# Performance work log

Measured on AMD Instinct MI355X. Metric: run time of the kernel, lower is better.

The kernel has to match this reference:

```python
import jax, jax.numpy as jnp
import numpy as np


def setup_inputs() -> dict:
    key = jax.random.key(0)
    k1, k2, k3 = jax.random.split(key, 3)
    B, N, D = 4, 256, 128
    s = jax.random.normal(k1, (B, N, D), dtype=jnp.float32)
    W1 = jax.random.normal(k2, (3 * D, 2 * D), dtype=jnp.float32) * 0.02
    b1 = jnp.zeros((2 * D,), dtype=jnp.float32)
    W2 = jax.random.normal(k3, (2 * D, 1), dtype=jnp.float32) * 0.02
    b2 = jnp.zeros((1,), dtype=jnp.float32)
    return {"s": s, "W1": W1, "b1": b1, "W2": W2, "b2": b2, "K": 8}


def reference(s, W1, b1, W2, b2, K):
    B, N, D = s.shape
    si = jnp.broadcast_to(s[:, :, None, :], (B, N, N, D))
    sj = jnp.broadcast_to(s[:, None, :, :], (B, N, N, D))
    pair = jnp.concatenate([si, sj, si * sj], axis=-1)  # [B,N,N,3D]
    h = jax.nn.relu(pair @ W1 + b1)                      # [B,N,N,2D]
    scores = (h @ W2 + b2)[..., 0]                       # [B,N,N]
    k = min(int(K), N)
    _, idx = jax.lax.top_k(scores, k)                    # [B,N,K]
    # scatter ones at topk indices (indices are distinct per row)
    gate = jnp.sum(jax.nn.one_hot(idx, N, dtype=jnp.float32), axis=-2)  # [B,N,N]
    w = gate / jnp.clip(jnp.sum(gate, axis=-1, keepdims=True), 1.0)
    ctx = jnp.einsum('bij,bjd->bid', w, s)               # [B,N,D]
    return ctx, gate, w
```

## Files before the change

kernel.cpp:

```cpp
#include <hip/hip_runtime.h>
#include <hip/hip_bf16.h>
#include <math.h>

#define B_ 4
#define N_ 256
#define D_ 128
#define H_ 256
#define K_ 8

typedef __attribute__((ext_vector_type(8))) short short8;
typedef __attribute__((ext_vector_type(4))) float f32x4;

__device__ __forceinline__ unsigned short f2bf(float x) {
    union { __hip_bfloat16 h; unsigned short s; } u;
    u.h = __float2bfloat16(x);
    return u.s;
}
__device__ __forceinline__ float bf2f(unsigned short b) {
    unsigned v = ((unsigned)b) << 16;
    return __builtin_bit_cast(float, v);
}
__device__ __forceinline__ unsigned pk2(float x, float y) {
    union { __hip_bfloat162 h; unsigned u; } c;
    c.h = __float22bfloat162_rn(float2{x, y});
    return c.u;
}
__device__ __forceinline__ void gld_lds16(const float* g, float* l) {
    __builtin_amdgcn_global_load_lds(
        (const __attribute__((address_space(1))) void*)g,
        (__attribute__((address_space(3))) void*)l, 16, 0, 0);
}

__global__ __launch_bounds__(256) void pre_kernel(
    const float* __restrict__ s, const float* __restrict__ W1,
    const float* __restrict__ b1,
    float* __restrict__ avec, float* __restrict__ bvec,
    unsigned short* __restrict__ Wt)
{
    int blk = blockIdx.x;
    int t = threadIdx.x;
    if (blk < 512) {
        int bi0 = blk * 2;
        __shared__ float s2[2][D_];
        {
            int r = t >> 7, d = t & 127;
            s2[r][d] = s[(size_t)(bi0 + r) * D_ + d];
        }
        __syncthreads();
        float aA0 = b1[t], aA1 = aA0, aB0 = 0.f, aB1 = 0.f;
        const float* W1a = W1 + t;
        const float* W1b = W1 + (size_t)D_ * H_ + t;
        #pragma unroll 8
        for (int d = 0; d < D_; ++d) {
            float wa = W1a[(size_t)d * H_];
            float wb = W1b[(size_t)d * H_];
            float s0 = s2[0][d], s1 = s2[1][d];
            aA0 = fmaf(s0, wa, aA0);
            aA1 = fmaf(s1, wa, aA1);
            aB0 = fmaf(s0, wb, aB0);
            aB1 = fmaf(s1, wb, aB1);
        }
        avec[(size_t)bi0 * H_ + t]       = aA0;
        avec[(size_t)(bi0 + 1) * H_ + t] = aA1;
        bvec[(size_t)bi0 * H_ + t]       = aB0;
        bvec[(size_t)(bi0 + 1) * H_ + t] = aB1;
    } else {
        int e = (blk - 512) * 256 + t;
        int h = e >> 7, d = e & 127;
        Wt[e] = f2bf(W1[(size_t)(2 * D_ + d) * H_ + h]);
    }
}

__global__ __launch_bounds__(512, 2) void approx_scores(
    const float* __restrict__ s, const unsigned short* __restrict__ Wt,
    const float* __restrict__ W2, const float* __restrict__ b2,
    const float* __restrict__ avec, const float* __restrict__ bvec,
    unsigned short* __restrict__ ascu)
{
    int blk = blockIdx.x;
    int b   = blk >> 6;
    int jtb = ((blk >> 4) & 3) * 64;
    int i0  = (blk & 15) * 16;
    int t = threadIdx.x;
    int lane = t & 63;
    int w = __builtin_amdgcn_readfirstlane(t >> 6);
    int l15 = lane & 15, quad = lane >> 4;

    __shared__ __align__(16) short Pl[2][64 * 128];
    __shared__ __align__(16) float si_all[16][D_];
    __shared__ float partial[2][8][64];

    const float* sB = s + (size_t)b * N_ * D_;

    {
        int ii = t >> 5, dq = t & 31;
        *(float4*)&si_all[ii][dq * 4] =
            *(const float4*)(sB + (size_t)(i0 + ii) * D_ + dq * 4);
    }

    short8 Wreg[2][4];
    #pragma unroll
    for (int mi = 0; mi < 2; ++mi)
        #pragma unroll
        for (int dk = 0; dk < 4; ++dk)
            Wreg[mi][dk] = *(const short8*)(
                Wt + (size_t)(w * 32 + mi * 16 + l15) * D_ + dk * 32 + quad * 8);
    float bvr[2][4][4];
    float w2r[2][4];
    #pragma unroll
    for (int mi = 0; mi < 2; ++mi) {
        int hq = w * 32 + mi * 16 + quad * 4;
        #pragma unroll
        for (int r = 0; r < 4; ++r)
            w2r[mi][r] = W2[hq + r];
        #pragma unroll
        for (int nj = 0; nj < 4; ++nj)
            #pragma unroll
            for (int r = 0; r < 4; ++r)
                bvr[mi][nj][r] = bvec[((size_t)(b * N_ + jtb + nj * 16 + l15)) * H_
                                      + hq + r];
    }
    float b2v = b2[0];
    __syncthreads();

    {
        int row = t >> 3, seg = t & 7;
        const float* sj = sB + (size_t)(jtb + row) * D_ + seg * 16;
        float4 a0 = ((const float4*)sj)[0], a1 = ((const float4*)sj)[1];
        float4 a2 = ((const float4*)sj)[2], a3 = ((const float4*)sj)[3];
        const float* si = &si_all[0][seg * 16];
        float4 s0 = ((const float4*)si)[0], s1 = ((const float4*)si)[1];
        float4 s2 = ((const float4*)si)[2], s3 = ((const float4*)si)[3];
        uint4 v0, v1;
        v0.x = pk2(a0.x * s0.x, a0.y * s0.y); v0.y = pk2(a0.z * s0.z, a0.w * s0.w);
        v0.z = pk2(a1.x * s1.x, a1.y * s1.y); v0.w = pk2(a1.z * s1.z, a1.w * s1.w);
        v1.x = pk2(a2.x * s2.x, a2.y * s2.y); v1.y = pk2(a2.z * s2.z, a2.w * s2.w);
        v1.z = pk2(a3.x * s3.x, a3.y * s3.y); v1.w = pk2(a3.z * s3.z, a3.w * s3.w);
        int pc0 = (seg * 2) ^ (row & 15), pc1 = (seg * 2 + 1) ^ (row & 15);
        *(uint4*)&Pl[0][row * 128 + pc0 * 8] = v0;
        *(uint4*)&Pl[0][row * 128 + pc1 * 8] = v1;
    }
    __syncthreads();

    #pragma unroll 1
    for (int i = 0; i < 16; ++i) {
        int cur = i & 1;
        if (w == 0 && i > 0) {
            float sum = b2v;
            #pragma unroll
            for (int ww = 0; ww < 8; ++ww) sum += partial[(i - 1) & 1][ww][lane];
            ascu[(size_t)(b * N_ + i0 + i - 1) * N_ + jtb + lane] = f2bf(sum);
        }
        float avc[2][4];
        #pragma unroll
        for (int mi = 0; mi < 2; ++mi) {
            int hq = w * 32 + mi * 16 + quad * 4;
            #pragma unroll
            for (int r = 0; r < 4; ++r)
                avc[mi][r] = avec[(size_t)(b * N_ + i0 + i) * H_ + hq + r];
        }
        f32x4 acc[2][4];
        #pragma unroll
        for (int mi = 0; mi < 2; ++mi)
            #pragma unroll
            for (int nj = 0; nj < 4; ++nj)
                acc[mi][nj] = (f32x4){0.f, 0.f, 0.f, 0.f};
        #pragma unroll
        for (int dk = 0; dk < 4; ++dk) {
            short8 Pf[4];
            #pragma unroll
            for (int nj = 0; nj < 4; ++nj) {
                int pcc = (dk * 4 + quad) ^ l15;
                Pf[nj] = *(const short8*)&Pl[cur][(nj * 16 + l15) * 128 + pcc * 8];
            }
            #pragma unroll
            for (int nj = 0; nj < 4; ++nj)
                #pragma unroll
                for (int mi = 0; mi < 2; ++mi)
                    acc[mi][nj] = __builtin_amdgcn_mfma_f32_16x16x32_bf16(
                        Wreg[mi][dk], Pf[nj], acc[mi][nj], 0, 0, 0);
        }
        if (i < 15) {
            int row = t >> 3, seg = t & 7;
            const float* sj = sB + (size_t)(jtb + row) * D_ + seg * 16;
            float4 a0 = ((const float4*)sj)[0], a1 = ((const float4*)sj)[1];
            float4 a2 = ((const float4*)sj)[2], a3 = ((const float4*)sj)[3];
            const float* si = &si_all[i + 1][seg * 16];
            float4 s0 = ((const float4*)si)[0], s1 = ((const float4*)si)[1];
            float4 s2 = ((const float4*)si)[2], s3 = ((const float4*)si)[3];
            uint4 v0, v1;
            v0.x = pk2(a0.x * s0.x, a0.y * s0.y); v0.y = pk2(a0.z * s0.z, a0.w * s0.w);
            v0.z = pk2(a1.x * s1.x, a1.y * s1.y); v0.w = pk2(a1.z * s1.z, a1.w * s1.w);
            v1.x = pk2(a2.x * s2.x, a2.y * s2.y); v1.y = pk2(a2.z * s2.z, a2.w * s2.w);
            v1.z = pk2(a3.x * s3.x, a3.y * s3.y); v1.w = pk2(a3.z * s3.z, a3.w * s3.w);
            int pc0 = (seg * 2) ^ (row & 15), pc1 = (seg * 2 + 1) ^ (row & 15);
            *(uint4*)&Pl[cur ^ 1][row * 128 + pc0 * 8] = v0;
            *(uint4*)&Pl[cur ^ 1][row * 128 + pc1 * 8] = v1;
        }
        float rs[4];
        #pragma unroll
        for (int nj = 0; nj < 4; ++nj) rs[nj] = 0.f;
        #pragma unroll
        for (int mi = 0; mi < 2; ++mi)
            #pragma unroll
            for (int nj = 0; nj < 4; ++nj)
                #pragma unroll
                for (int r = 0; r < 4; ++r) {
                    float z = acc[mi][nj][r] + avc[mi][r] + bvr[mi][nj][r];
                    rs[nj] = fmaf(fmaxf(z, 0.f), w2r[mi][r], rs[nj]);
                }
        #pragma unroll
        for (int nj = 0; nj < 4; ++nj) {
            rs[nj] += __shfl_xor(rs[nj], 16);
            rs[nj] += __shfl_xor(rs[nj], 32);
        }
        float v = (quad == 0) ? rs[0] : (quad == 1) ? rs[1] : (quad == 2) ? rs[2] : rs[3];
        partial[cur][w][lane] = v;
        __syncthreads();
    }
    if (w == 0) {
        float sum = b2v;
        #pragma unroll
        for (int ww = 0; ww < 8; ++ww) sum += partial[15 & 1][ww][lane];
        ascu[(size_t)(b * N_ + i0 + 15) * N_ + jtb + lane] = f2bf(sum);
    }
}

#define DC2 16
#define PADT 17
__global__ __launch_bounds__(256) void finalize_kernel(
    const float* __restrict__ s, const float* __restrict__ W1,
    const float* __restrict__ W2, const float* __restrict__ b2,
    const float* __restrict__ avec, const float* __restrict__ bvec,
    const unsigned short* __restrict__ ascu,
    float* __restrict__ ctx, float* __restrict__ gate, float* __restrict__ w)
{
    int bi = blockIdx.x;
    int b = bi >> 8;
    int t = threadIdx.x;

    __shared__ float asc[N_];
    __shared__ int cand[16];
    __shared__ __align__(16) float Pt[D_][PADT];
    __shared__ __align__(16) float Wl[2][DC2 * H_];
    __shared__ float part[16][17];
    __shared__ float rsc[16];
    __shared__ int sel8[8];

    asc[t] = bf2f(ascu[(size_t)bi * N_ + t]);
    __syncthreads();
    {
        float my = asc[t];
        int rank = 0;
        #pragma unroll 8
        for (int j2 = 0; j2 < N_; ++j2) {
            float o = asc[j2];
            rank += (o > my) || (o == my && j2 < t);
        }
        if (rank < 16) cand[rank] = t;
    }
    __syncthreads();

    const float* Wc = W1 + (size_t)2 * D_ * H_;

    #pragma unroll
    for (int k = 0; k < 4; ++k) {
        int slot = t + 256 * k;
        gld_lds16(Wc + slot * 4, &Wl[0][slot * 4]);
    }

    for (int e = t; e < 512; e += 256) {
        int c = e & 15, dq = e >> 4;
        int j = cand[c];
        float4 sj = *(const float4*)(s + ((size_t)(b * N_ + j)) * D_ + dq * 4);
        float4 si = *(const float4*)(s + (size_t)bi * D_ + dq * 4);
        Pt[dq * 4 + 0][c] = si.x * sj.x;
        Pt[dq * 4 + 1][c] = si.y * sj.y;
        Pt[dq * 4 + 2][c] = si.z * sj.z;
        Pt[dq * 4 + 3][c] = si.w * sj.w;
    }

    int c = t & 15, hg = t >> 4;
    int h0 = hg * 16;
    int jc = cand[c];
    float acc[16];
    {
        const float* av = avec + (size_t)bi * H_ + h0;
        const float* bv = bvec + ((size_t)(b * N_ + jc)) * H_ + h0;
        #pragma unroll
        for (int m4 = 0; m4 < 4; ++m4) {
            float4 a4 = *(const float4*)(av + m4 * 4);
            float4 b4 = *(const float4*)(bv + m4 * 4);
            acc[m4 * 4 + 0] = a4.x + b4.x;
            acc[m4 * 4 + 1] = a4.y + b4.y;
            acc[m4 * 4 + 2] = a4.z + b4.z;
            acc[m4 * 4 + 3] = a4.w + b4.w;
        }
    }
    __syncthreads();

    #pragma unroll 1
    for (int ch = 0; ch < 8; ++ch) {
        int cur = ch & 1;
        if (ch < 7) {
            const float* src = Wc + (size_t)(ch + 1) * DC2 * H_;
            #pragma unroll
            for (int k = 0; k < 4; ++k) {
                int slot = t + 256 * k;
                gld_lds16(src + slot * 4, &Wl[cur ^ 1][slot * 4]);
            }
        }
        int d0 = ch * DC2;
        #pragma unroll
        for (int d = 0; d < DC2; ++d) {
            float pv = Pt[d0 + d][c];
            float wv[16];
            *(float4*)&wv[0]  = *(const float4*)&Wl[cur][d * H_ + h0];
            *(float4*)&wv[4]  = *(const float4*)&Wl[cur][d * H_ + h0 + 4];
            *(float4*)&wv[8]  = *(const float4*)&Wl[cur][d * H_ + h0 + 8];
            *(float4*)&wv[12] = *(const float4*)&Wl[cur][d * H_ + h0 + 12];
            #pragma unroll
            for (int m = 0; m < 16; ++m)
                acc[m] = fmaf(pv, wv[m], acc[m]);
        }
        __syncthreads();
    }

    {
        float w2v[16];
        *(float4*)&w2v[0]  = *(const float4*)(W2 + h0);
        *(float4*)&w2v[4]  = *(const float4*)(W2 + h0 + 4);
        *(float4*)&w2v[8]  = *(const float4*)(W2 + h0 + 8);
        *(float4*)&w2v[12] = *(const float4*)(W2 + h0 + 12);
        float sc = 0.f;
        #pragma unroll
        for (int m = 0; m < 16; ++m)
            sc = fmaf(fmaxf(acc[m], 0.f), w2v[m], sc);
        part[c][hg] = sc;
    }
    __syncthreads();
    if (t < 16) {
        float sum = b2[0];
        #pragma unroll
        for (int m = 0; m < 16; ++m) sum += part[t][m];
        rsc[t] = sum;
    }
    __syncthreads();

    if (t < 16) {
        float my = rsc[t]; int myj = cand[t];
        int rank = 0;
        #pragma unroll
        for (int c2 = 0; c2 < 16; ++c2) {
            float o = rsc[c2]; int oj = cand[c2];
            rank += (o > my) || (o == my && oj < myj);
        }
        if (rank < 8) sel8[rank] = myj;
    }
    __syncthreads();

    {
        float gv = 0.f;
        #pragma unroll
        for (int m = 0; m < 8; ++m)
            gv = (t == sel8[m]) ? 1.f : gv;
        gate[(size_t)bi * N_ + t] = gv;
        w[(size_t)bi * N_ + t]    = gv * 0.125f;
    }
    if (t < 128) {
        float a = 0.f;
        #pragma unroll
        for (int m = 0; m < 8; ++m)
            a += s[((size_t)(b * N_ + sel8[m])) * D_ + t];
        ctx[(size_t)bi * D_ + t] = a * 0.125f;
    }
}

extern "C" void kernel_launch(void* const* d_in, const int* in_sizes, int n_in,
                              void* d_out, int out_size, void* d_ws, size_t ws_size,
                              hipStream_t stream)
{
    const float* s  = (const float*)d_in[0];
    const float* W1 = (const float*)d_in[1];
    const float* b1 = (const float*)d_in[2];
    const float* W2 = (const float*)d_in[3];
    const float* b2 = (const float*)d_in[4];

    float* avec = (float*)d_ws;
    float* bvec = avec + (size_t)B_ * N_ * H_;
    unsigned short* ascu = (unsigned short*)(bvec + (size_t)B_ * N_ * H_);
    unsigned short* Wtu  = ascu + (size_t)B_ * N_ * N_;

    float* ctx  = (float*)d_out;
    float* gate = ctx + (size_t)B_ * N_ * D_;
    float* wout = gate + (size_t)B_ * N_ * N_;

    pre_kernel<<<640, 256, 0, stream>>>(s, W1, b1, avec, bvec, Wtu);
    approx_scores<<<256, 512, 0, stream>>>(s, Wtu, W2, b2, avec, bvec, ascu);
    finalize_kernel<<<B_ * N_, 256, 0, stream>>>(s, W1, W2, b2, avec, bvec, ascu,
                                                 ctx, gate, wout);
}
```

Before: 141.7 us.

## Process four rows per finalize block to reuse staged W1 chunks

```diff
diff --git a/kernel.cpp b/kernel.cpp
--- a/kernel.cpp
+++ b/kernel.cpp
@@ -227,7 +227,7 @@
 }
 
 #define DC2 16
-#define PADT 17
+#define PTRS 2064
 __global__ __launch_bounds__(256) void finalize_kernel(
     const float* __restrict__ s, const float* __restrict__ W1,
     const float* __restrict__ W2, const float* __restrict__ b2,
@@ -235,29 +235,41 @@
     const unsigned short* __restrict__ ascu,
     float* __restrict__ ctx, float* __restrict__ gate, float* __restrict__ w)
 {
-    int bi = blockIdx.x;
-    int b = bi >> 8;
+    int bi0 = blockIdx.x * 4;
+    int b = bi0 >> 8;
     int t = threadIdx.x;
 
-    __shared__ float asc[N_];
-    __shared__ int cand[16];
-    __shared__ __align__(16) float Pt[D_][PADT];
+    __shared__ float asc[4][N_];
+    __shared__ int cand[4][16];
+    __shared__ __align__(16) float Pt[4 * PTRS];
     __shared__ __align__(16) float Wl[2][DC2 * H_];
-    __shared__ float part[16][17];
-    __shared__ float rsc[16];
-    __shared__ int sel8[8];
-
-    asc[t] = bf2f(ascu[(size_t)bi * N_ + t]);
-    __syncthreads();
+    __shared__ float part[4][16][17];
+    __shared__ float rsc[4][16];
+    __shared__ int sel8[4][8];
+
+    for (int e = t; e < 1024; e += 256) {
+        int r = e >> 8, jj = e & 255;
+        asc[r][jj] = bf2f(ascu[(size_t)(bi0 + r) * N_ + jj]);
+    }
+    __syncthreads();
+
     {
-        float my = asc[t];
-        int rank = 0;
-        #pragma unroll 8
+        int r = t >> 6, lj = t & 63;
+        float my[4]; int rk[4];
+        #pragma unroll
+        for (int m = 0; m < 4; ++m) { my[m] = asc[r][m * 64 + lj]; rk[m] = 0; }
+        #pragma unroll 4
         for (int j2 = 0; j2 < N_; ++j2) {
-            float o = asc[j2];
-            rank += (o > my) || (o == my && j2 < t);
-        }
-        if (rank < 16) cand[rank] = t;
+            float o = asc[r][j2];
+            #pragma unroll
+            for (int m = 0; m < 4; ++m) {
+                int jm = m * 64 + lj;
+                rk[m] += (o > my[m]) || (o == my[m] && j2 < jm);
+            }
+        }
+        #pragma unroll
+        for (int m = 0; m < 4; ++m)
+            if (rk[m] < 16) cand[r][rk[m]] = m * 64 + lj;
     }
     __syncthreads();
 
@@ -269,36 +281,45 @@
         gld_lds16(Wc + slot * 4, &Wl[0][slot * 4]);
     }
 
-    for (int e = t; e < 512; e += 256) {
-        int c = e & 15, dq = e >> 4;
-        int j = cand[c];
+    for (int e = t; e < 2048; e += 256) {
+        int rr = e >> 9, c = (e >> 5) & 15, dq = e & 31;
+        int j = cand[rr][c];
         float4 sj = *(const float4*)(s + ((size_t)(b * N_ + j)) * D_ + dq * 4);
-        float4 si = *(const float4*)(s + (size_t)bi * D_ + dq * 4);
-        Pt[dq * 4 + 0][c] = si.x * sj.x;
-        Pt[dq * 4 + 1][c] = si.y * sj.y;
-        Pt[dq * 4 + 2][c] = si.z * sj.z;
-        Pt[dq * 4 + 3][c] = si.w * sj.w;
-    }
-
-    int c = t & 15, hg = t >> 4;
+        float4 si = *(const float4*)(s + ((size_t)(bi0 + rr)) * D_ + dq * 4);
+        int pc = ((c >> 2) ^ rr) & 3;
+        int base = rr * PTRS + (dq * 4) * 16 + pc * 4 + (c & 3);
+        Pt[base + 0 * 16] = si.x * sj.x;
+        Pt[base + 1 * 16] = si.y * sj.y;
+        Pt[base + 2 * 16] = si.z * sj.z;
+        Pt[base + 3 * 16] = si.w * sj.w;
+    }
+
+    int cg = t & 3, rr = (t >> 2) & 3;
+    int hg = (t >> 6) * 4 + ((t >> 4) & 3);
     int h0 = hg * 16;
-    int jc = cand[c];
-    float acc[16];
+    float acc[4][16];
     {
-        const float* av = avec + (size_t)bi * H_ + h0;
-        const float* bv = bvec + ((size_t)(b * N_ + jc)) * H_ + h0;
-        #pragma unroll
-        for (int m4 = 0; m4 < 4; ++m4) {
-            float4 a4 = *(const float4*)(av + m4 * 4);
-            float4 b4 = *(const float4*)(bv + m4 * 4);
-            acc[m4 * 4 + 0] = a4.x + b4.x;
-            acc[m4 * 4 + 1] = a4.y + b4.y;
-            acc[m4 * 4 + 2] = a4.z + b4.z;
-            acc[m4 * 4 + 3] = a4.w + b4.w;
-        }
-    }
-    __syncthreads();
-
+        const float* av = avec + (size_t)(bi0 + rr) * H_ + h0;
+        float4 av4[4];
+        #pragma unroll
+        for (int m4 = 0; m4 < 4; ++m4) av4[m4] = *(const float4*)(av + m4 * 4);
+        #pragma unroll
+        for (int cc = 0; cc < 4; ++cc) {
+            int j = cand[rr][cg * 4 + cc];
+            const float* bv = bvec + ((size_t)(b * N_ + j)) * H_ + h0;
+            #pragma unroll
+            for (int m4 = 0; m4 < 4; ++m4) {
+                float4 b4 = *(const float4*)(bv + m4 * 4);
+                acc[cc][m4 * 4 + 0] = av4[m4].x + b4.x;
+                acc[cc][m4 * 4 + 1] = av4[m4].y + b4.y;
+                acc[cc][m4 * 4 + 2] = av4[m4].z + b4.z;
+                acc[cc][m4 * 4 + 3] = av4[m4].w + b4.w;
+            }
+        }
+    }
+    __syncthreads();
+
+    int pvoff = rr * PTRS + ((cg ^ rr) & 3) * 4;
     #pragma unroll 1
     for (int ch = 0; ch < 8; ++ch) {
         int cur = ch & 1;
@@ -313,15 +334,19 @@
         int d0 = ch * DC2;
         #pragma unroll
         for (int d = 0; d < DC2; ++d) {
-            float pv = Pt[d0 + d][c];
+            float4 pv = *(const float4*)&Pt[pvoff + (d0 + d) * 16];
             float wv[16];
             *(float4*)&wv[0]  = *(const float4*)&Wl[cur][d * H_ + h0];
             *(float4*)&wv[4]  = *(const float4*)&Wl[cur][d * H_ + h0 + 4];
             *(float4*)&wv[8]  = *(const float4*)&Wl[cur][d * H_ + h0 + 8];
             *(float4*)&wv[12] = *(const float4*)&Wl[cur][d * H_ + h0 + 12];
             #pragma unroll
-            for (int m = 0; m < 16; ++m)
-                acc[m] = fmaf(pv, wv[m], acc[m]);
+            for (int m = 0; m < 16; ++m) {
+                acc[0][m] = fmaf(pv.x, wv[m], acc[0][m]);
+                acc[1][m] = fmaf(pv.y, wv[m], acc[1][m]);
+                acc[2][m] = fmaf(pv.z, wv[m], acc[2][m]);
+                acc[3][m] = fmaf(pv.w, wv[m], acc[3][m]);
+            }
         }
         __syncthreads();
     }
@@ -332,47 +357,54 @@
         *(float4*)&w2v[4]  = *(const float4*)(W2 + h0 + 4);
         *(float4*)&w2v[8]  = *(const float4*)(W2 + h0 + 8);
         *(float4*)&w2v[12] = *(const float4*)(W2 + h0 + 12);
-        float sc = 0.f;
-        #pragma unroll
-        for (int m = 0; m < 16; ++m)
-            sc = fmaf(fmaxf(acc[m], 0.f), w2v[m], sc);
-        part[c][hg] = sc;
-    }
-    __syncthreads();
-    if (t < 16) {
+        #pragma unroll
+        for (int cc = 0; cc < 4; ++cc) {
+            float sc = 0.f;
+            #pragma unroll
+            for (int m = 0; m < 16; ++m)
+                sc = fmaf(fmaxf(acc[cc][m], 0.f), w2v[m], sc);
+            part[rr][cg * 4 + cc][hg] = sc;
+        }
+    }
+    __syncthreads();
+    if (t < 64) {
+        int r2 = t >> 4, c2 = t & 15;
         float sum = b2[0];
         #pragma unroll
-        for (int m = 0; m < 16; ++m) sum += part[t][m];
-        rsc[t] = sum;
-    }
-    __syncthreads();
-
-    if (t < 16) {
-        float my = rsc[t]; int myj = cand[t];
+        for (int m = 0; m < 16; ++m) sum += part[r2][c2][m];
+        rsc[r2][c2] = sum;
+    }
+    __syncthreads();
+
+    if (t < 64) {
+        int r2 = t >> 4, c2 = t & 15;
+        float my = rsc[r2][c2]; int myj = cand[r2][c2];
         int rank = 0;
         #pragma unroll
-        for (int c2 = 0; c2 < 16; ++c2) {
-            float o = rsc[c2]; int oj = cand[c2];
+        for (int c3 = 0; c3 < 16; ++c3) {
+            float o = rsc[r2][c3]; int oj = cand[r2][c3];
             rank += (o > my) || (o == my && oj < myj);
         }
-        if (rank < 8) sel8[rank] = myj;
-    }
-    __syncthreads();
-
-    {
+        if (rank < 8) sel8[r2][rank] = myj;
+    }
+    __syncthreads();
+
+    for (int e = t; e < 1024; e += 256) {
+        int r2 = e >> 8, jj = e & 255;
         float gv = 0.f;
         #pragma unroll
         for (int m = 0; m < 8; ++m)
-            gv = (t == sel8[m]) ? 1.f : gv;
-        gate[(size_t)bi * N_ + t] = gv;
-        w[(size_t)bi * N_ + t]    = gv * 0.125f;
-    }
-    if (t < 128) {
+            gv = (jj == sel8[r2][m]) ? 1.f : gv;
+        gate[(size_t)(bi0 + r2) * N_ + jj] = gv;
+        w[(size_t)(bi0 + r2) * N_ + jj]    = gv * 0.125f;
+    }
+    for (int e = t; e < 512; e += 256) {
+        int r2 = e >> 7, d = e & 127;
         float a = 0.f;
         #pragma unroll
         for (int m = 0; m < 8; ++m)
-            a += s[((size_t)(b * N_ + sel8[m])) * D_ + t];
-        ctx[(size_t)bi * D_ + t] = a * 0.125f;
+            a += s[((size_t)(b * N_ + sel8[r2][m])) * D_ + d];
+        ctx[(size_t)(bi0 + r2) * D_ + d] = a * 0.125f;
     }
 }
 
@@ -397,6 +429,6 @@
 
     pre_kernel<<<640, 256, 0, stream>>>(s, W1, b1, avec, bvec, Wtu);
     approx_scores<<<256, 512, 0, stream>>>(s, Wtu, W2, b2, avec, bvec, ascu);
-    finalize_kernel<<<B_ * N_, 256, 0, stream>>>(s, W1, W2, b2, avec, bvec, ascu,
-                                                 ctx, gate, wout);
-}
+    finalize_kernel<<<B_ * N_ / 4, 256, 0, stream>>>(s, W1, W2, b2, avec, bvec, ascu,
+                                                     ctx, gate, wout);
+}
```

Measured after the change: 147.9 us. +4.4%, slower.
